# Kernel tuning notes

Hardware: AMD Instinct MI355X
Metric: run time of the kernel (lower is better)

The kernel has to match this reference:

```python
import jax, jax.numpy as jnp
import numpy as np

EMBED_DIM = 1024
N_HEAD = 16
BLOCK_SIZE = 2048
B, T = 4, 2048


def setup_inputs() -> dict:
    key = jax.random.key(0)
    kx, kw, kb = jax.random.split(key, 3)
    x = jax.random.normal(kx, (B, T, EMBED_DIM), dtype=jnp.float32)
    # nn.Linear(embed_dim, 3*embed_dim): weight [3C, C], bias [3C]
    bound = 1.0 / np.sqrt(EMBED_DIM)
    W_qkv = jax.random.uniform(kw, (3 * EMBED_DIM, EMBED_DIM), dtype=jnp.float32, minval=-bound, maxval=bound)
    b_qkv = jax.random.uniform(kb, (3 * EMBED_DIM,), dtype=jnp.float32, minval=-bound, maxval=bound)
    return {"x": x, "W_qkv": W_qkv, "b_qkv": b_qkv}


def reference(x, W_qkv, b_qkv):
    Bsz, Tlen, C = x.shape
    H = N_HEAD
    hd = C // H
    qkv = x @ W_qkv.T + b_qkv  # [B, T, 3C]
    q, k, v = jnp.split(qkv, 3, axis=2)
    # [B, H, T, hd]
    q = q.reshape(Bsz, Tlen, H, hd).transpose(0, 2, 1, 3)
    k = k.reshape(Bsz, Tlen, H, hd).transpose(0, 2, 1, 3)
    v = v.reshape(Bsz, Tlen, H, hd).transpose(0, 2, 1, 3)
    att = jnp.einsum('bhqd,bhkd->bhqk', q, k) / np.sqrt(hd).astype(np.float32)
    causal = jnp.tril(jnp.ones((Tlen, Tlen), dtype=bool))
    att = jnp.where(causal[None, None, :, :], att, -jnp.inf)
    att = jax.nn.softmax(att, axis=-1)
    out = jnp.einsum('bhqk,bhkd->bhqd', att, v)  # [B, H, T, hd]
    y = out.transpose(0, 2, 1, 3).reshape(Bsz, Tlen, C)
    return y
```

## Files before the change

### kernel.cpp

```cpp
#include <hip/hip_runtime.h>


typedef unsigned short u16;
typedef short bf16x8 __attribute__((ext_vector_type(8)));
typedef float f32x4 __attribute__((ext_vector_type(4)));
typedef float f32x16 __attribute__((ext_vector_type(16)));

__device__ __forceinline__ float exp2f_hw(float x) {
  return __builtin_amdgcn_exp2f(x);
}

__device__ __forceinline__ u16 f2b(float f) {
  union { float f; unsigned u; } x; x.f = f;
  unsigned r = x.u + 0x7FFFu + ((x.u >> 16) & 1u);
  return (u16)(r >> 16);
}

__device__ __forceinline__ unsigned cvtpk(float lo, float hi_) {
  unsigned r;
  asm("v_cvt_pk_bf16_f32 %0, %1, %2" : "=v"(r) : "v"(lo), "v"(hi_));
  return r;
}

__device__ __forceinline__ void gload16(const void* g, void* l) {
  __builtin_amdgcn_global_load_lds(
      (const __attribute__((address_space(1))) unsigned*)g,
      (__attribute__((address_space(3))) unsigned*)l, 16, 0, 0);
}

__global__ void cvt_bf16(const float* __restrict__ src, u16* __restrict__ dst, int n4) {
  int i = blockIdx.x * blockDim.x + threadIdx.x;
  const int stride = gridDim.x * blockDim.x;
  for (; i < n4; i += stride) {
    float4 v = ((const float4*)src)[i];
    ushort4 o;
    o.x = f2b(v.x); o.y = f2b(v.y); o.z = f2b(v.z); o.w = f2b(v.w);
    ((ushort4*)dst)[i] = o;
  }
}

__global__ __launch_bounds__(256) void qkv_gemm(
    const u16* __restrict__ Xb, const u16* __restrict__ Wb,
    const float* __restrict__ bias,
    u16* __restrict__ qw, u16* __restrict__ kw, u16* __restrict__ vw) {
  __shared__ u16 As[128 * 32];
  __shared__ u16 Bs[128 * 32];
  const int tid  = threadIdx.x;
  const int lane = tid & 63;
  const int wave = tid >> 6;
  const int ln = lane & 15, hi = lane >> 4;
  const int wr = wave >> 1, wc = wave & 1;
  const int m0 = blockIdx.y * 128;
  const int n0 = blockIdx.x * 128;
  const bool vblk = (n0 >= 2048);

  const int srow = tid >> 2;
  const int scol = (tid & 3) * 8;

  f32x4 zero = {0.f, 0.f, 0.f, 0.f};
  f32x4 acc[4][4];
#pragma unroll
  for (int i = 0; i < 4; ++i)
#pragma unroll
    for (int j = 0; j < 4; ++j) acc[i][j] = zero;

  for (int k0 = 0; k0 < 1024; k0 += 32) {
    gload16(Xb + (size_t)(m0 + srow) * 1024 + k0 + scol,      (char*)As + tid * 16);
    gload16(Xb + (size_t)(m0 + 64 + srow) * 1024 + k0 + scol, (char*)As + 4096 + tid * 16);
    gload16(Wb + (size_t)(n0 + srow) * 1024 + k0 + scol,      (char*)Bs + tid * 16);
    gload16(Wb + (size_t)(n0 + 64 + srow) * 1024 + k0 + scol, (char*)Bs + 4096 + tid * 16);
    __syncthreads();

    bf16x8 af[4], bfv[4];
#pragma unroll
    for (int i = 0; i < 4; ++i)
      af[i] = *(const bf16x8*)&As[(wr * 64 + i * 16 + ln) * 32 + hi * 8];
#pragma unroll
    for (int j = 0; j < 4; ++j)
      bfv[j] = *(const bf16x8*)&Bs[(wc * 64 + j * 16 + ln) * 32 + hi * 8];
    if (vblk) {
#pragma unroll
      for (int i = 0; i < 4; ++i)
#pragma unroll
        for (int j = 0; j < 4; ++j)
          acc[i][j] = __builtin_amdgcn_mfma_f32_16x16x32_bf16(bfv[j], af[i], acc[i][j], 0, 0, 0);
    } else {
#pragma unroll
      for (int i = 0; i < 4; ++i)
#pragma unroll
        for (int j = 0; j < 4; ++j)
          acc[i][j] = __builtin_amdgcn_mfma_f32_16x16x32_bf16(af[i], bfv[j], acc[i][j], 0, 0, 0);
    }
    __syncthreads();
  }

  const int which = n0 >> 10;
  const int h = ((n0 & 1023) >> 6) + wc;
  const size_t bh = (size_t)((m0 >> 11) * 16 + h);
  const int tloc = (m0 & 2047) + wr * 64;

  if (which == 2) {
    u16* ob = vw + bh * 131072;
#pragma unroll
    for (int j = 0; j < 4; ++j) {
      float bv[4];
#pragma unroll
      for (int r = 0; r < 4; ++r) bv[r] = bias[n0 + wc * 64 + j * 16 + hi * 4 + r];
#pragma unroll
      for (int i = 0; i < 4; ++i) {
        u16* p = ob + (((tloc >> 4) + i) * 64 + j * 16 + hi * 4) * 16 + ln;
#pragma unroll
        for (int r = 0; r < 4; ++r)
          p[r * 16] = f2b(acc[i][j][r] + bv[r]);
      }
    }
  } else {
    u16* ob = (which == 0 ? qw : kw) + bh * 131072;
    const float qs = (which == 0) ? 0.1803368801111244f : 1.0f;
    const int t5 = tloc >> 5;
#pragma unroll
    for (int j = 0; j < 4; ++j) {
      const float bv = bias[n0 + wc * 64 + j * 16 + ln];
#pragma unroll
      for (int i = 0; i < 4; ++i) {
        u16* p = ob + ((t5 + (i >> 1)) * 4 + j) * 512 + ((i & 1) * 16 + hi * 4) * 16 + ln;
#pragma unroll
        for (int r = 0; r < 4; ++r)
          p[r * 16] = f2b((acc[i][j][r] + bv) * qs);
      }
    }
  }
}

__global__ __launch_bounds__(256) void attn(
    const u16* __restrict__ qw, const u16* __restrict__ kw,
    const u16* __restrict__ vw, float* __restrict__ y) {
  __shared__ float accX[2][2][16][64];
  __shared__ float mlX[2][2][2][64];

  const int lane = threadIdx.x & 63;
  const int wave = threadIdx.x >> 6;
  const int l31 = lane & 31;
  const int hi  = lane >> 5;
  const int pairI = wave >> 1;
  const int p     = wave & 1;
  const int laneoff = l31 * 16 + hi * 8;

  const int bid = blockIdx.x;
  const int xcd = bid & 7;
  const int rest = bid >> 3;
  const int blk = rest & 15;
  const int bh  = xcd + 8 * (rest >> 4);
  const int bb  = bh >> 4, h = bh & 15;
  const int task = 2 * blk + pairI;

  const u16* qb = qw + (size_t)bh * 131072;
  const u16* kb = kw + (size_t)bh * 131072;
  const u16* vb = vw + (size_t)bh * 131072;
  float* yb = y + (size_t)bb * 2048 * 1024 + (size_t)h * 64;

#pragma unroll 1
  for (int phase = 0; phase < 2; ++phase) {
    const int chunk = phase ? (63 - task) : task;
    const int q0 = chunk * 32;
    const int jtE = chunk;

    bf16x8 qf[4];
#pragma unroll
    for (int s = 0; s < 4; ++s)
      qf[s] = *(const bf16x8*)&qb[(chunk * 4 + s) * 512 + laneoff];

    f32x16 acc0, acc1;
#pragma unroll
    for (int r = 0; r < 16; ++r) { acc0[r] = 0.f; acc1[r] = 0.f; }
    float mrow = -1e30f, lrow = 0.f;

    bf16x8 kfA[4], kfB[4];
#pragma unroll
    for (int s = 0; s < 4; ++s)
      kfA[s] = *(const bf16x8*)&kb[(p * 4 + s) * 512 + laneoff];

    int tog = 0;
#pragma unroll 1
    for (int jt = p; jt <= jtE; jt += 2) {
      bf16x8 vf[4];
      vf[0] = *(const bf16x8*)&vb[((jt * 2 + 0) * 64 +  0 + l31) * 16 + hi * 8];
      vf[1] = *(const bf16x8*)&vb[((jt * 2 + 0) * 64 + 32 + l31) * 16 + hi * 8];
      vf[2] = *(const bf16x8*)&vb[((jt * 2 + 1) * 64 +  0 + l31) * 16 + hi * 8];
      vf[3] = *(const bf16x8*)&vb[((jt * 2 + 1) * 64 + 32 + l31) * 16 + hi * 8];

      f32x16 st;
#pragma unroll
      for (int r = 0; r < 16; ++r) st[r] = 0.f;
      if (tog == 0) {
        if (jt + 2 <= jtE) {
#pragma unroll
          for (int s = 0; s < 4; ++s)
            kfB[s] = *(const bf16x8*)&kb[((jt + 2) * 4 + s) * 512 + laneoff];
        }
#pragma unroll
        for (int s = 0; s < 4; ++s)
          st = __builtin_amdgcn_mfma_f32_32x32x16_bf16(kfA[s], qf[s], st, 0, 0, 0);
      } else {
        if (jt + 2 <= jtE) {
#pragma unroll
          for (int s = 0; s < 4; ++s)
            kfA[s] = *(const bf16x8*)&kb[((jt + 2) * 4 + s) * 512 + laneoff];
        }
#pragma unroll
        for (int s = 0; s < 4; ++s)
          st = __builtin_amdgcn_mfma_f32_32x32x16_bf16(kfB[s], qf[s], st, 0, 0, 0);
      }
      tog ^= 1;

      if (jt == jtE) {
#pragma unroll
        for (int r = 0; r < 16; ++r) {
          const int crow = (r & 3) + 8 * (r >> 2) + 4 * hi;
          if (crow > l31) st[r] = -1e30f;
        }
      }

      float m0 = fmaxf(fmaxf(fmaxf(st[0], st[1]), fmaxf(st[2], st[3])),
                       fmaxf(fmaxf(st[4], st[5]), fmaxf(st[6], st[7])));
      float m1 = fmaxf(fmaxf(fmaxf(st[8], st[9]), fmaxf(st[10], st[11])),
                       fmaxf(fmaxf(st[12], st[13]), fmaxf(st[14], st[15])));
      float mt = fmaxf(m0, m1);
      mt = fmaxf(mt, __shfl_xor(mt, 32));

      if (__any(mt > mrow + 8.f)) {
        const float mn = fmaxf(mrow, mt);
        const float al = exp2f_hw(mrow - mn);
        mrow = mn;
        lrow *= al;
#pragma unroll
        for (int r = 0; r < 16; ++r) {
          const float ar = __shfl(al, (r & 3) + 8 * (r >> 2) + 4 * hi);
          acc0[r] *= ar; acc1[r] *= ar;
        }
      }

#pragma unroll
      for (int r = 0; r < 16; ++r) st[r] = exp2f_hw(st[r] - mrow);
      float p0 = ((st[0] + st[1]) + (st[2] + st[3])) + ((st[4] + st[5]) + (st[6] + st[7]));
      float p1 = ((st[8] + st[9]) + (st[10] + st[11])) + ((st[12] + st[13]) + (st[14] + st[15]));
      float ps = p0 + p1;
      ps += __shfl_xor(ps, 32);
      lrow += ps;

      bf16x8 pa0, pa1;
      {
        unsigned x0 = cvtpk(st[0], st[1]),  y0 = cvtpk(st[4], st[5]);
        unsigned x1 = cvtpk(st[2], st[3]),  y1 = cvtpk(st[6], st[7]);
        auto s0 = __builtin_amdgcn_permlane32_swap(x0, y0, false, false);
        auto s1 = __builtin_amdgcn_permlane32_swap(x1, y1, false, false);
        union { unsigned w[4]; bf16x8 v; } u;
        u.w[0] = s0[0]; u.w[1] = s1[0]; u.w[2] = s0[1]; u.w[3] = s1[1];
        pa0 = u.v;
      }
      {
        unsigned x0 = cvtpk(st[8], st[9]),   y0 = cvtpk(st[12], st[13]);
        unsigned x1 = cvtpk(st[10], st[11]), y1 = cvtpk(st[14], st[15]);
        auto s0 = __builtin_amdgcn_permlane32_swap(x0, y0, false, false);
        auto s1 = __builtin_amdgcn_permlane32_swap(x1, y1, false, false);
        union { unsigned w[4]; bf16x8 v; } u;
        u.w[0] = s0[0]; u.w[1] = s1[0]; u.w[2] = s0[1]; u.w[3] = s1[1];
        pa1 = u.v;
      }

      acc0 = __builtin_amdgcn_mfma_f32_32x32x16_bf16(pa0, vf[0], acc0, 0, 0, 0);
      acc1 = __builtin_amdgcn_mfma_f32_32x32x16_bf16(pa0, vf[1], acc1, 0, 0, 0);
      acc0 = __builtin_amdgcn_mfma_f32_32x32x16_bf16(pa1, vf[2], acc0, 0, 0, 0);
      acc1 = __builtin_amdgcn_mfma_f32_32x32x16_bf16(pa1, vf[3], acc1, 0, 0, 0);
    }

    __syncthreads();
    if (p == 0) {
#pragma unroll
      for (int r = 0; r < 16; ++r) accX[pairI][0][r][lane] = acc1[r];
      mlX[pairI][0][0][lane] = mrow;
      mlX[pairI][0][1][lane] = lrow;
    } else {
#pragma unroll
      for (int r = 0; r < 16; ++r) accX[pairI][1][r][lane] = acc0[r];
      mlX[pairI][1][0][lane] = mrow;
      mlX[pairI][1][1][lane] = lrow;
    }
    __syncthreads();

    const float mo = mlX[pairI][p ^ 1][0][lane];
    const float lo = mlX[pairI][p ^ 1][1][lane];
    const float mm = fmaxf(mrow, mo);
    const float sS = exp2f_hw(mrow - mm);
    const float sO = exp2f_hw(mo - mm);
    const float inv = 1.0f / (lrow * sS + lo * sO);
    const float fa = sS * inv, fb = sO * inv;

#pragma unroll
    for (int r = 0; r < 16; ++r) {
      const int crow = (r & 3) + 8 * (r >> 2) + 4 * hi;
      const float ga = __shfl(fa, crow);
      const float gb = __shfl(fb, crow);
      const float own = (p == 0) ? acc0[r] : acc1[r];
      const float oth = accX[pairI][p ^ 1][r][lane];
      yb[(size_t)(q0 + crow) * 1024 + p * 32 + l31] = own * ga + oth * gb;
    }
  }
}

extern "C" void kernel_launch(void* const* d_in, const int* in_sizes, int n_in,
                              void* d_out, int out_size, void* d_ws, size_t ws_size,
                              hipStream_t stream) {
  const float* x    = (const float*)d_in[0];
  const float* W    = (const float*)d_in[1];
  const float* bias = (const float*)d_in[2];
  float* y = (float*)d_out;

  char* ws = (char*)d_ws;
  u16* xb = (u16*)(ws);
  u16* Wb = (u16*)(ws + 16777216);
  u16* qw = (u16*)(ws + 23068672);
  u16* kw = (u16*)(ws + 39845888);
  u16* vw = (u16*)(ws + 56623104);

  cvt_bf16<<<2048, 256, 0, stream>>>(x, xb, 8388608 / 4);
  cvt_bf16<<<1024, 256, 0, stream>>>(W, Wb, 3145728 / 4);
  qkv_gemm<<<dim3(24, 64), 256, 0, stream>>>(xb, Wb, bias, qw, kw, vw);
  attn<<<1024, 256, 0, stream>>>(qw, kw, vw, y);
}
```

Baseline: 161.5 us.

## Double GEMM K-step, split attention into 2-wave blocks, use permlane reductions

The QKV GEMM now stages 64 K-elements per iteration, which halves the number of barrier pairs. The cost is doubled LDS tiles. The attention kernel moves from 256-thread blocks holding two wave-pairs to 128-thread blocks holding one pair, launched twice as many times. This should allow finer scheduling and smaller per-block LDS. The K-fragment double-buffering toggle is replaced by a single buffer reloaded after the QK MFMAs, and the cross-half max/sum reductions switch from __shfl_xor to permlane32_swap, trading some prefetch overlap for fewer registers and cheaper cross-lane ops.

Measured after the change: 155.6 us. -3.6%, faster.

```diff
diff --git a/kernel.cpp b/kernel.cpp
--- a/kernel.cpp
+++ b/kernel.cpp
@@ -20,6 +20,17 @@
   unsigned r;
   asm("v_cvt_pk_bf16_f32 %0, %1, %2" : "=v"(r) : "v"(lo), "v"(hi_));
   return r;
+}
+
+__device__ __forceinline__ float pair_max(float v) {
+  unsigned a = __float_as_uint(v);
+  auto s = __builtin_amdgcn_permlane32_swap(a, a, false, false);
+  return fmaxf(__uint_as_float(s[0]), __uint_as_float(s[1]));
+}
+__device__ __forceinline__ float pair_sum(float v) {
+  unsigned a = __float_as_uint(v);
+  auto s = __builtin_amdgcn_permlane32_swap(a, a, false, false);
+  return __uint_as_float(s[0]) + __uint_as_float(s[1]);
 }
 
 __device__ __forceinline__ void gload16(const void* g, void* l) {
@@ -43,8 +54,8 @@
     const u16* __restrict__ Xb, const u16* __restrict__ Wb,
     const float* __restrict__ bias,
     u16* __restrict__ qw, u16* __restrict__ kw, u16* __restrict__ vw) {
-  __shared__ u16 As[128 * 32];
-  __shared__ u16 Bs[128 * 32];
+  __shared__ u16 As[8192];
+  __shared__ u16 Bs[8192];
   const int tid  = threadIdx.x;
   const int lane = tid & 63;
   const int wave = tid >> 6;
@@ -64,32 +75,41 @@
 #pragma unroll
     for (int j = 0; j < 4; ++j) acc[i][j] = zero;
 
-  for (int k0 = 0; k0 < 1024; k0 += 32) {
-    gload16(Xb + (size_t)(m0 + srow) * 1024 + k0 + scol,      (char*)As + tid * 16);
-    gload16(Xb + (size_t)(m0 + 64 + srow) * 1024 + k0 + scol, (char*)As + 4096 + tid * 16);
-    gload16(Wb + (size_t)(n0 + srow) * 1024 + k0 + scol,      (char*)Bs + tid * 16);
-    gload16(Wb + (size_t)(n0 + 64 + srow) * 1024 + k0 + scol, (char*)Bs + 4096 + tid * 16);
+  for (int k0 = 0; k0 < 1024; k0 += 64) {
+    gload16(Xb + (size_t)(m0 + srow) * 1024 + k0 + scol,           (char*)As + tid * 16);
+    gload16(Xb + (size_t)(m0 + 64 + srow) * 1024 + k0 + scol,      (char*)As + 4096 + tid * 16);
+    gload16(Xb + (size_t)(m0 + srow) * 1024 + k0 + 32 + scol,      (char*)As + 8192 + tid * 16);
+    gload16(Xb + (size_t)(m0 + 64 + srow) * 1024 + k0 + 32 + scol, (char*)As + 12288 + tid * 16);
+    gload16(Wb + (size_t)(n0 + srow) * 1024 + k0 + scol,           (char*)Bs + tid * 16);
+    gload16(Wb + (size_t)(n0 + 64 + srow) * 1024 + k0 + scol,      (char*)Bs + 4096 + tid * 16);
+    gload16(Wb + (size_t)(n0 + srow) * 1024 + k0 + 32 + scol,      (char*)Bs + 8192 + tid * 16);
+    gload16(Wb + (size_t)(n0 + 64 + srow) * 1024 + k0 + 32 + scol, (char*)Bs + 12288 + tid * 16);
     __syncthreads();
 
-    bf16x8 af[4], bfv[4];
-#pragma unroll
-    for (int i = 0; i < 4; ++i)
-      af[i] = *(const bf16x8*)&As[(wr * 64 + i * 16 + ln) * 32 + hi * 8];
-#pragma unroll
-    for (int j = 0; j < 4; ++j)
-      bfv[j] = *(const bf16x8*)&Bs[(wc * 64 + j * 16 + ln) * 32 + hi * 8];
-    if (vblk) {
+#pragma unroll
+    for (int hf = 0; hf < 2; ++hf) {
+      const u16* Ah = As + hf * 4096;
+      const u16* Bh = Bs + hf * 4096;
+      bf16x8 af[4], bfv[4];
 #pragma unroll
       for (int i = 0; i < 4; ++i)
-#pragma unroll
-        for (int j = 0; j < 4; ++j)
-          acc[i][j] = __builtin_amdgcn_mfma_f32_16x16x32_bf16(bfv[j], af[i], acc[i][j], 0, 0, 0);
-    } else {
-#pragma unroll
-      for (int i = 0; i < 4; ++i)
-#pragma unroll
-        for (int j = 0; j < 4; ++j)
-          acc[i][j] = __builtin_amdgcn_mfma_f32_16x16x32_bf16(af[i], bfv[j], acc[i][j], 0, 0, 0);
+        af[i] = *(const bf16x8*)&Ah[(wr * 64 + i * 16 + ln) * 32 + hi * 8];
+#pragma unroll
+      for (int j = 0; j < 4; ++j)
+        bfv[j] = *(const bf16x8*)&Bh[(wc * 64 + j * 16 + ln) * 32 + hi * 8];
+      if (vblk) {
+#pragma unroll
+        for (int i = 0; i < 4; ++i)
+#pragma unroll
+          for (int j = 0; j < 4; ++j)
+            acc[i][j] = __builtin_amdgcn_mfma_f32_16x16x32_bf16(bfv[j], af[i], acc[i][j], 0, 0, 0);
+      } else {
+#pragma unroll
+        for (int i = 0; i < 4; ++i)
+#pragma unroll
+          for (int j = 0; j < 4; ++j)
+            acc[i][j] = __builtin_amdgcn_mfma_f32_16x16x32_bf16(af[i], bfv[j], acc[i][j], 0, 0, 0);
+      }
     }
     __syncthreads();
   }
@@ -132,27 +152,24 @@
   }
 }
 
-__global__ __launch_bounds__(256) void attn(
+__global__ __launch_bounds__(128) void attn(
     const u16* __restrict__ qw, const u16* __restrict__ kw,
     const u16* __restrict__ vw, float* __restrict__ y) {
-  __shared__ float accX[2][2][16][64];
-  __shared__ float mlX[2][2][2][64];
+  __shared__ float accX[2][16][64];
+  __shared__ float mlX[2][2][64];
 
   const int lane = threadIdx.x & 63;
-  const int wave = threadIdx.x >> 6;
+  const int p    = threadIdx.x >> 6;
   const int l31 = lane & 31;
   const int hi  = lane >> 5;
-  const int pairI = wave >> 1;
-  const int p     = wave & 1;
   const int laneoff = l31 * 16 + hi * 8;
 
   const int bid = blockIdx.x;
   const int xcd = bid & 7;
   const int rest = bid >> 3;
-  const int blk = rest & 15;
-  const int bh  = xcd + 8 * (rest >> 4);
+  const int task = rest & 31;
+  const int bh  = xcd + 8 * (rest >> 5);
   const int bb  = bh >> 4, h = bh & 15;
-  const int task = 2 * blk + pairI;
 
   const u16* qb = qw + (size_t)bh * 131072;
   const u16* kb = kw + (size_t)bh * 131072;
@@ -175,12 +192,11 @@
     for (int r = 0; r < 16; ++r) { acc0[r] = 0.f; acc1[r] = 0.f; }
     float mrow = -1e30f, lrow = 0.f;
 
-    bf16x8 kfA[4], kfB[4];
+    bf16x8 kf[4];
 #pragma unroll
     for (int s = 0; s < 4; ++s)
-      kfA[s] = *(const bf16x8*)&kb[(p * 4 + s) * 512 + laneoff];
-
-    int tog = 0;
+      kf[s] = *(const bf16x8*)&kb[(p * 4 + s) * 512 + laneoff];
+
 #pragma unroll 1
     for (int jt = p; jt <= jtE; jt += 2) {
       bf16x8 vf[4];
@@ -192,26 +208,15 @@
       f32x16 st;
 #pragma unroll
       for (int r = 0; r < 16; ++r) st[r] = 0.f;
-      if (tog == 0) {
-        if (jt + 2 <= jtE) {
-#pragma unroll
-          for (int s = 0; s < 4; ++s)
-            kfB[s] = *(const bf16x8*)&kb[((jt + 2) * 4 + s) * 512 + laneoff];
-        }
+#pragma unroll
+      for (int s = 0; s < 4; ++s)
+        st = __builtin_amdgcn_mfma_f32_32x32x16_bf16(kf[s], qf[s], st, 0, 0, 0);
+
+      if (jt + 2 <= jtE) {
 #pragma unroll
         for (int s = 0; s < 4; ++s)
-          st = __builtin_amdgcn_mfma_f32_32x32x16_bf16(kfA[s], qf[s], st, 0, 0, 0);
-      } else {
-        if (jt + 2 <= jtE) {
-#pragma unroll
-          for (int s = 0; s < 4; ++s)
-            kfA[s] = *(const bf16x8*)&kb[((jt + 2) * 4 + s) * 512 + laneoff];
-        }
-#pragma unroll
-        for (int s = 0; s < 4; ++s)
-          st = __builtin_amdgcn_mfma_f32_32x32x16_bf16(kfB[s], qf[s], st, 0, 0, 0);
-      }
-      tog ^= 1;
+          kf[s] = *(const bf16x8*)&kb[((jt + 2) * 4 + s) * 512 + laneoff];
+      }
 
       if (jt == jtE) {
 #pragma unroll
@@ -221,12 +226,11 @@
         }
       }
 
-      float m0 = fmaxf(fmaxf(fmaxf(st[0], st[1]), fmaxf(st[2], st[3])),
-                       fmaxf(fmaxf(st[4], st[5]), fmaxf(st[6], st[7])));
-      float m1 = fmaxf(fmaxf(fmaxf(st[8], st[9]), fmaxf(st[10], st[11])),
-                       fmaxf(fmaxf(st[12], st[13]), fmaxf(st[14], st[15])));
-      float mt = fmaxf(m0, m1);
-      mt = fmaxf(mt, __shfl_xor(mt, 32));
+      float m0_ = fmaxf(fmaxf(fmaxf(st[0], st[1]), fmaxf(st[2], st[3])),
+                        fmaxf(fmaxf(st[4], st[5]), fmaxf(st[6], st[7])));
+      float m1_ = fmaxf(fmaxf(fmaxf(st[8], st[9]), fmaxf(st[10], st[11])),
+                        fmaxf(fmaxf(st[12], st[13]), fmaxf(st[14], st[15])));
+      const float mt = pair_max(fmaxf(m0_, m1_));
 
       if (__any(mt > mrow + 8.f)) {
         const float mn = fmaxf(mrow, mt);
@@ -244,9 +248,7 @@
       for (int r = 0; r < 16; ++r) st[r] = exp2f_hw(st[r] - mrow);
       float p0 = ((st[0] + st[1]) + (st[2] + st[3])) + ((st[4] + st[5]) + (st[6] + st[7]));
       float p1 = ((st[8] + st[9]) + (st[10] + st[11])) + ((st[12] + st[13]) + (st[14] + st[15]));
-      float ps = p0 + p1;
-      ps += __shfl_xor(ps, 32);
-      lrow += ps;
+      lrow += pair_sum(p0 + p1);
 
       bf16x8 pa0, pa1;
       {
@@ -277,19 +279,19 @@
     __syncthreads();
     if (p == 0) {
 #pragma unroll
-      for (int r = 0; r < 16; ++r) accX[pairI][0][r][lane] = acc1[r];
-      mlX[pairI][0][0][lane] = mrow;
-      mlX[pairI][0][1][lane] = lrow;
+      for (int r = 0; r < 16; ++r) accX[0][r][lane] = acc1[r];
+      mlX[0][0][lane] = mrow;
+      mlX[0][1][lane] = lrow;
     } else {
 #pragma unroll
-      for (int r = 0; r < 16; ++r) accX[pairI][1][r][lane] = acc0[r];
-      mlX[pairI][1][0][lane] = mrow;
-      mlX[pairI][1][1][lane] = lrow;
+      for (int r = 0; r < 16; ++r) accX[1][r][lane] = acc0[r];
+      mlX[1][0][lane] = mrow;
+      mlX[1][1][lane] = lrow;
     }
     __syncthreads();
 
-    const float mo = mlX[pairI][p ^ 1][0][lane];
-    const float lo = mlX[pairI][p ^ 1][1][lane];
+    const float mo = mlX[p ^ 1][0][lane];
+    const float lo = mlX[p ^ 1][1][lane];
     const float mm = fmaxf(mrow, mo);
     const float sS = exp2f_hw(mrow - mm);
     const float sO = exp2f_hw(mo - mm);
@@ -302,7 +304,7 @@
       const float ga = __shfl(fa, crow);
       const float gb = __shfl(fb, crow);
       const float own = (p == 0) ? acc0[r] : acc1[r];
-      const float oth = accX[pairI][p ^ 1][r][lane];
+      const float oth = accX[p ^ 1][r][lane];
       yb[(size_t)(q0 + crow) * 1024 + p * 32 + l31] = own * ga + oth * gb;
     }
   }
@@ -326,5 +328,5 @@
   cvt_bf16<<<2048, 256, 0, stream>>>(x, xb, 8388608 / 4);
   cvt_bf16<<<1024, 256, 0, stream>>>(W, Wb, 3145728 / 4);
   qkv_gemm<<<dim3(24, 64), 256, 0, stream>>>(xb, Wb, bias, qw, kw, vw);
-  attn<<<1024, 256, 0, stream>>>(qw, kw, vw, y);
-}
+  attn<<<2048, 128, 0, stream>>>(qw, kw, vw, y);
+}
```
